# Optimization experiments

Hardware: AMD Instinct MI355X
Metric: run time of the kernel (lower is better)

## Reference

```python
import jax, jax.numpy as jnp
import numpy as np

GRAVITY = 9.81
W_INERTIA = 1.0
W_GRAVITY = 0.01
W_STRAIN = 1.0

V = 500_000
E = 2_000_000


def setup_inputs() -> dict:
    key = jax.random.key(0)
    ks = jax.random.split(key, 7)
    pos_next = jax.random.normal(ks[0], (V, 3), dtype=jnp.float32)
    pos_curr = jax.random.normal(ks[1], (V, 3), dtype=jnp.float32)
    pos_prev = jax.random.normal(ks[2], (V, 3), dtype=jnp.float32)
    mass = jax.random.uniform(ks[3], (V, 1), dtype=jnp.float32)
    elements = jax.random.randint(ks[4], (E, 4), 0, V, dtype=jnp.int64)
    rest_volumes = jax.random.uniform(ks[5], (E,), dtype=jnp.float32)
    rest_inv = jax.random.normal(ks[6], (E, 3, 3), dtype=jnp.float32)
    lam = jnp.float32(1.0)
    mu = jnpp_one = jnp.float32(1.0)
    return {
        "pos_next": pos_next, "pos_curr": pos_curr, "pos_prev": pos_prev,
        "mass": mass, "elements": elements, "rest_volumes": rest_volumes,
        "rest_inv": rest_inv, "lam": lam, "mu": mu,
    }


def _det3(F):
    # F: (E, 3, 3)
    return (F[:, 0, 0] * (F[:, 1, 1] * F[:, 2, 2] - F[:, 1, 2] * F[:, 2, 1])
            - F[:, 0, 1] * (F[:, 1, 0] * F[:, 2, 2] - F[:, 1, 2] * F[:, 2, 0])
            + F[:, 0, 2] * (F[:, 1, 0] * F[:, 2, 1] - F[:, 1, 1] * F[:, 2, 0]))


def _physics_loss(pos_next, pos_curr, pos_prev, mass, elements, rest_volumes, rest_inv, lam, mu):
    # Inertia: mean over all V*3 entries of 0.5 * m * a^2
    accel = pos_next + pos_prev - 2.0 * pos_curr          # (V, 3)
    inertia = 0.5 * jnp.mean(mass * accel * accel)
    # Gravity: -mean(m * g * y)
    gravity = -jnp.mean(mass * GRAVITY * pos_curr[:, 1:2])
    # Strain (Neo-Hookean) on pos_next
    v = pos_next[elements]                                 # (E, 4, 3)
    Ds = jnp.stack([v[:, 1] - v[:, 0], v[:, 2] - v[:, 0], v[:, 3] - v[:, 0]], axis=-1)  # (E,3,3)
    F_def = jnp.einsum('eij,ejk->eik', Ds, rest_inv)       # (E, 3, 3)
    det_F = jnp.maximum(_det3(F_def), 1e-8)
    log_det = jnp.log(det_F)
    tr_FtF = jnp.sum(F_def * F_def, axis=(1, 2))           # trace(F^T F) = ||F||_F^2
    psi = 0.5 * lam * log_det ** 2 - mu * log_det + 0.5 * mu * (tr_FtF - 3.0)
    strain = jnp.mean(psi * rest_volumes)
    return W_INERTIA * inertia + W_GRAVITY * gravity + W_STRAIN * strain


def reference(pos_next, pos_curr, pos_prev, mass, elements, rest_volumes, rest_inv, lam, mu):
    return _physics_loss(pos_next, pos_curr, pos_prev, mass, elements, rest_volumes, rest_inv, lam, mu)
```

## Files before the change

### kernel.cpp

```cpp
#include <hip/hip_runtime.h>

#define GRAVITY_F 9.81f

__device__ __forceinline__ float blockReduceSum(float val) {
    #pragma unroll
    for (int off = 32; off > 0; off >>= 1)
        val += __shfl_down(val, off, 64);
    __shared__ float smem[16];
    const int lane = threadIdx.x & 63;
    const int wave = threadIdx.x >> 6;
    if (lane == 0) smem[wave] = val;
    __syncthreads();
    const int nwaves = (blockDim.x + 63) >> 6;
    val = 0.0f;
    if (wave == 0) {
        if (lane < nwaves) val = smem[lane];
        #pragma unroll
        for (int off = 8; off > 0; off >>= 1)
            val += __shfl_down(val, off, 64);
    }
    return val;
}

__global__ void fused_kernel(const float* __restrict__ pn,
                             const float* __restrict__ pc,
                             const float* __restrict__ pp,
                             const float* __restrict__ mass,
                             const int*   __restrict__ elems,
                             const float* __restrict__ vols,
                             const float* __restrict__ rinv,
                             const float* __restrict__ lam_p,
                             const float* __restrict__ mu_p,
                             float* __restrict__ partials,
                             double* __restrict__ acc,
                             int V, int E,
                             float sI, float sG, float sS) {
    const int i = blockIdx.x * blockDim.x + threadIdx.x;
    float local = 0.0f;

    if (i < V) {
        const int v = i;
        const float m  = mass[v];
        const float p0 = pc[3 * v + 0];
        const float y  = pc[3 * v + 1];
        const float p2 = pc[3 * v + 2];
        const float a0 = pn[3 * v + 0] + pp[3 * v + 0] - 2.0f * p0;
        const float a1 = pn[3 * v + 1] + pp[3 * v + 1] - 2.0f * y;
        const float a2 = pn[3 * v + 2] + pp[3 * v + 2] - 2.0f * p2;
        local = sI * (m * (a0 * a0 + a1 * a1 + a2 * a2)) + sG * (m * y);
    } else if (i < V + E) {
        const int e = i - V;
        const float lam = lam_p[0];
        const float mu  = mu_p[0];
        const int4 idx = ((const int4*)elems)[e];
        const float* v0 = pn + 3 * (size_t)idx.x;
        const float* v1 = pn + 3 * (size_t)idx.y;
        const float* v2 = pn + 3 * (size_t)idx.z;
        const float* v3 = pn + 3 * (size_t)idx.w;

        float d[3][3];
        #pragma unroll
        for (int r = 0; r < 3; ++r) {
            const float b = v0[r];
            d[r][0] = v1[r] - b;
            d[r][1] = v2[r] - b;
            d[r][2] = v3[r] - b;
        }

        const float* R = rinv + 9 * (size_t)e;
        float F[3][3];
        #pragma unroll
        for (int r = 0; r < 3; ++r) {
            #pragma unroll
            for (int k = 0; k < 3; ++k) {
                F[r][k] = d[r][0] * R[0 * 3 + k]
                        + d[r][1] * R[1 * 3 + k]
                        + d[r][2] * R[2 * 3 + k];
            }
        }

        const float det = F[0][0] * (F[1][1] * F[2][2] - F[1][2] * F[2][1])
                        - F[0][1] * (F[1][0] * F[2][2] - F[1][2] * F[2][0])
                        + F[0][2] * (F[1][0] * F[2][1] - F[1][1] * F[2][0]);
        const float ld = logf(fmaxf(det, 1e-8f));
        float tr = 0.0f;
        #pragma unroll
        for (int r = 0; r < 3; ++r)
            #pragma unroll
            for (int k = 0; k < 3; ++k)
                tr += F[r][k] * F[r][k];

        const float psi = 0.5f * lam * ld * ld - mu * ld + 0.5f * mu * (tr - 3.0f);
        local = sS * (psi * vols[e]);
    }

    const float tot = blockReduceSum(local);
    if (threadIdx.x == 0) {
        if (partials) partials[blockIdx.x] = tot;
        else atomicAdd(acc, (double)tot);
    }
}

__global__ void reduce_kernel(const float* __restrict__ partials, int n,
                              float* __restrict__ out) {
    double s = 0.0;
    for (int i = threadIdx.x; i < n; i += blockDim.x)
        s += (double)partials[i];
    __shared__ double sm[256];
    sm[threadIdx.x] = s;
    __syncthreads();
    #pragma unroll
    for (int off = 128; off > 0; off >>= 1) {
        if (threadIdx.x < off) sm[threadIdx.x] += sm[threadIdx.x + off];
        __syncthreads();
    }
    if (threadIdx.x == 0) out[0] = (float)sm[0];
}

__global__ void init_acc_kernel(double* acc) {
    if (threadIdx.x == 0 && blockIdx.x == 0) acc[0] = 0.0;
}
__global__ void finalize_kernel(const double* __restrict__ acc,
                                float* __restrict__ out) {
    if (threadIdx.x == 0 && blockIdx.x == 0) out[0] = (float)acc[0];
}

extern "C" void kernel_launch(void* const* d_in, const int* in_sizes, int n_in,
                              void* d_out, int out_size, void* d_ws, size_t ws_size,
                              hipStream_t stream) {
    const float* pos_next = (const float*)d_in[0];
    const float* pos_curr = (const float*)d_in[1];
    const float* pos_prev = (const float*)d_in[2];
    const float* mass     = (const float*)d_in[3];
    const int*   elements = (const int*)d_in[4];
    const float* rest_vol = (const float*)d_in[5];
    const float* rest_inv = (const float*)d_in[6];
    const float* lam_p    = (const float*)d_in[7];
    const float* mu_p     = (const float*)d_in[8];
    float* out = (float*)d_out;

    const int V = in_sizes[3];
    const int E = in_sizes[5];

    const float sI = 0.5f / (3.0f * (float)V);
    const float sG = -0.01f * GRAVITY_F / (float)V;
    const float sS = 1.0f / (float)E;

    const int block = 256;
    const int nitems = V + E;
    const int grid = (nitems + block - 1) / block;

    const bool use_partials = ws_size >= (size_t)grid * sizeof(float) + 64;

    if (use_partials) {
        float* partials = (float*)d_ws;
        fused_kernel<<<grid, block, 0, stream>>>(pos_next, pos_curr, pos_prev,
                                                 mass, elements, rest_vol,
                                                 rest_inv, lam_p, mu_p,
                                                 partials, nullptr,
                                                 V, E, sI, sG, sS);
        reduce_kernel<<<1, 256, 0, stream>>>(partials, grid, out);
    } else {
        double* acc = (double*)d_ws;
        init_acc_kernel<<<1, 1, 0, stream>>>(acc);
        fused_kernel<<<grid, block, 0, stream>>>(pos_next, pos_curr, pos_prev,
                                                 mass, elements, rest_vol,
                                                 rest_inv, lam_p, mu_p,
                                                 nullptr, acc,
                                                 V, E, sI, sG, sS);
        finalize_kernel<<<1, 1, 0, stream>>>(acc, out);
    }
}
```

Baseline: 229.9 us.

## Split blocks by role, process two elements per thread, use nontemporal streaming loads

Vertex and element work now go to separate, block-aligned ranges, so no wave is split between the two paths. Each element-block thread handles two tetrahedra and issues both index loads before computing, which raises memory-level parallelism for the gathers. Streaming inputs (mass, pos_curr, pos_prev, indices, volumes, rest_inv) use nontemporal loads so they do not evict pos_next from cache, since pos_next is gathered. The atomic fallback path is removed, so the code now assumes the workspace is large enough to hold the per-block partials.

```diff
diff --git a/kernel.cpp b/kernel.cpp
--- a/kernel.cpp
+++ b/kernel.cpp
@@ -1,6 +1,8 @@
 #include <hip/hip_runtime.h>
 
 #define GRAVITY_F 9.81f
+
+typedef int v4i __attribute__((ext_vector_type(4)));
 
 __device__ __forceinline__ float blockReduceSum(float val) {
     #pragma unroll
@@ -22,6 +24,51 @@
     return val;
 }
 
+__device__ __forceinline__ float elem_term(const float* __restrict__ pn,
+                                           const v4i idx,
+                                           const float vol,
+                                           const float* __restrict__ R,
+                                           float lam, float mu, float sS) {
+    float x0[3], x1[3], x2[3], x3[3];
+    const float* v0 = pn + 3 * (size_t)idx.x;
+    const float* v1 = pn + 3 * (size_t)idx.y;
+    const float* v2 = pn + 3 * (size_t)idx.z;
+    const float* v3 = pn + 3 * (size_t)idx.w;
+    #pragma unroll
+    for (int r = 0; r < 3; ++r) { x0[r] = v0[r]; x1[r] = v1[r]; x2[r] = v2[r]; x3[r] = v3[r]; }
+
+    float Rv[9];
+    #pragma unroll
+    for (int k = 0; k < 9; ++k) Rv[k] = __builtin_nontemporal_load(R + k);
+
+    float d[3][3];
+    #pragma unroll
+    for (int r = 0; r < 3; ++r) {
+        d[r][0] = x1[r] - x0[r];
+        d[r][1] = x2[r] - x0[r];
+        d[r][2] = x3[r] - x0[r];
+    }
+    float F[3][3];
+    #pragma unroll
+    for (int r = 0; r < 3; ++r) {
+        #pragma unroll
+        for (int k = 0; k < 3; ++k)
+            F[r][k] = d[r][0] * Rv[0 * 3 + k] + d[r][1] * Rv[1 * 3 + k] + d[r][2] * Rv[2 * 3 + k];
+    }
+    const float det = F[0][0] * (F[1][1] * F[2][2] - F[1][2] * F[2][1])
+                    - F[0][1] * (F[1][0] * F[2][2] - F[1][2] * F[2][0])
+                    + F[0][2] * (F[1][0] * F[2][1] - F[1][1] * F[2][0]);
+    const float ld = logf(fmaxf(det, 1e-8f));
+    float tr = 0.0f;
+    #pragma unroll
+    for (int r = 0; r < 3; ++r)
+        #pragma unroll
+        for (int k = 0; k < 3; ++k)
+            tr += F[r][k] * F[r][k];
+    const float psi = 0.5f * lam * ld * ld - mu * ld + 0.5f * mu * (tr - 3.0f);
+    return sS * (psi * vol);
+}
+
 __global__ void fused_kernel(const float* __restrict__ pn,
                              const float* __restrict__ pc,
                              const float* __restrict__ pp,
@@ -32,73 +79,48 @@
                              const float* __restrict__ lam_p,
                              const float* __restrict__ mu_p,
                              float* __restrict__ partials,
-                             double* __restrict__ acc,
-                             int V, int E,
+                             int V, int E, int Vblocks,
                              float sI, float sG, float sS) {
-    const int i = blockIdx.x * blockDim.x + threadIdx.x;
     float local = 0.0f;
 
-    if (i < V) {
-        const int v = i;
-        const float m  = mass[v];
-        const float p0 = pc[3 * v + 0];
-        const float y  = pc[3 * v + 1];
-        const float p2 = pc[3 * v + 2];
-        const float a0 = pn[3 * v + 0] + pp[3 * v + 0] - 2.0f * p0;
-        const float a1 = pn[3 * v + 1] + pp[3 * v + 1] - 2.0f * y;
-        const float a2 = pn[3 * v + 2] + pp[3 * v + 2] - 2.0f * p2;
-        local = sI * (m * (a0 * a0 + a1 * a1 + a2 * a2)) + sG * (m * y);
-    } else if (i < V + E) {
-        const int e = i - V;
+    if ((int)blockIdx.x < Vblocks) {
+        const int v = blockIdx.x * blockDim.x + threadIdx.x;
+        if (v < V) {
+            const float m  = __builtin_nontemporal_load(mass + v);
+            const float p0 = __builtin_nontemporal_load(pc + 3 * v + 0);
+            const float y  = __builtin_nontemporal_load(pc + 3 * v + 1);
+            const float p2 = __builtin_nontemporal_load(pc + 3 * v + 2);
+            const float n0 = pn[3 * v + 0];
+            const float n1 = pn[3 * v + 1];
+            const float n2 = pn[3 * v + 2];
+            const float q0 = __builtin_nontemporal_load(pp + 3 * v + 0);
+            const float q1 = __builtin_nontemporal_load(pp + 3 * v + 1);
+            const float q2 = __builtin_nontemporal_load(pp + 3 * v + 2);
+            const float a0 = n0 + q0 - 2.0f * p0;
+            const float a1 = n1 + q1 - 2.0f * y;
+            const float a2 = n2 + q2 - 2.0f * p2;
+            local = sI * (m * (a0 * a0 + a1 * a1 + a2 * a2)) + sG * (m * y);
+        }
+    } else {
         const float lam = lam_p[0];
         const float mu  = mu_p[0];
-        const int4 idx = ((const int4*)elems)[e];
-        const float* v0 = pn + 3 * (size_t)idx.x;
-        const float* v1 = pn + 3 * (size_t)idx.y;
-        const float* v2 = pn + 3 * (size_t)idx.z;
-        const float* v3 = pn + 3 * (size_t)idx.w;
+        const int base = (blockIdx.x - Vblocks) * (2 * blockDim.x);
+        const int e0 = base + threadIdx.x;
+        const int e1 = e0 + blockDim.x;
 
-        float d[3][3];
-        #pragma unroll
-        for (int r = 0; r < 3; ++r) {
-            const float b = v0[r];
-            d[r][0] = v1[r] - b;
-            d[r][1] = v2[r] - b;
-            d[r][2] = v3[r] - b;
-        }
-
-        const float* R = rinv + 9 * (size_t)e;
-        float F[3][3];
-        #pragma unroll
-        for (int r = 0; r < 3; ++r) {
-            #pragma unroll
-            for (int k = 0; k < 3; ++k) {
-                F[r][k] = d[r][0] * R[0 * 3 + k]
-                        + d[r][1] * R[1 * 3 + k]
-                        + d[r][2] * R[2 * 3 + k];
-            }
-        }
-
-        const float det = F[0][0] * (F[1][1] * F[2][2] - F[1][2] * F[2][1])
-                        - F[0][1] * (F[1][0] * F[2][2] - F[1][2] * F[2][0])
-                        + F[0][2] * (F[1][0] * F[2][1] - F[1][1] * F[2][0]);
-        const float ld = logf(fmaxf(det, 1e-8f));
-        float tr = 0.0f;
-        #pragma unroll
-        for (int r = 0; r < 3; ++r)
-            #pragma unroll
-            for (int k = 0; k < 3; ++k)
-                tr += F[r][k] * F[r][k];
-
-        const float psi = 0.5f * lam * ld * ld - mu * ld + 0.5f * mu * (tr - 3.0f);
-        local = sS * (psi * vols[e]);
+        v4i idx0 = (v4i)(0), idx1 = (v4i)(0);
+        float vol0 = 0.0f, vol1 = 0.0f;
+        const bool ok0 = e0 < E, ok1 = e1 < E;
+        if (ok0) { idx0 = __builtin_nontemporal_load(((const v4i*)elems) + e0);
+                   vol0 = __builtin_nontemporal_load(vols + e0); }
+        if (ok1) { idx1 = __builtin_nontemporal_load(((const v4i*)elems) + e1);
+                   vol1 = __builtin_nontemporal_load(vols + e1); }
+        if (ok0) local += elem_term(pn, idx0, vol0, rinv + 9 * (size_t)e0, lam, mu, sS);
+        if (ok1) local += elem_term(pn, idx1, vol1, rinv + 9 * (size_t)e1, lam, mu, sS);
     }
 
     const float tot = blockReduceSum(local);
-    if (threadIdx.x == 0) {
-        if (partials) partials[blockIdx.x] = tot;
-        else atomicAdd(acc, (double)tot);
-    }
+    if (threadIdx.x == 0) partials[blockIdx.x] = tot;
 }
 
 __global__ void reduce_kernel(const float* __restrict__ partials, int n,
@@ -115,14 +137,6 @@
         __syncthreads();
     }
     if (threadIdx.x == 0) out[0] = (float)sm[0];
-}
-
-__global__ void init_acc_kernel(double* acc) {
-    if (threadIdx.x == 0 && blockIdx.x == 0) acc[0] = 0.0;
-}
-__global__ void finalize_kernel(const double* __restrict__ acc,
-                                float* __restrict__ out) {
-    if (threadIdx.x == 0 && blockIdx.x == 0) out[0] = (float)acc[0];
 }
 
 extern "C" void kernel_launch(void* const* d_in, const int* in_sizes, int n_in,
@@ -147,27 +161,16 @@
     const float sS = 1.0f / (float)E;
 
     const int block = 256;
-    const int nitems = V + E;
-    const int grid = (nitems + block - 1) / block;
+    const int Vblocks = (V + block - 1) / block;
+    const int Eblocks = (E + 2 * block - 1) / (2 * block);
+    const int grid = Vblocks + Eblocks;
 
-    const bool use_partials = ws_size >= (size_t)grid * sizeof(float) + 64;
+    float* partials = (float*)d_ws;
 
-    if (use_partials) {
-        float* partials = (float*)d_ws;
-        fused_kernel<<<grid, block, 0, stream>>>(pos_next, pos_curr, pos_prev,
-                                                 mass, elements, rest_vol,
-                                                 rest_inv, lam_p, mu_p,
-                                                 partials, nullptr,
-                                                 V, E, sI, sG, sS);
-        reduce_kernel<<<1, 256, 0, stream>>>(partials, grid, out);
-    } else {
-        double* acc = (double*)d_ws;
-        init_acc_kernel<<<1, 1, 0, stream>>>(acc);
-        fused_kernel<<<grid, block, 0, stream>>>(pos_next, pos_curr, pos_prev,
-                                                 mass, elements, rest_vol,
-                                                 rest_inv, lam_p, mu_p,
-                                                 nullptr, acc,
-                                                 V, E, sI, sG, sS);
-        finalize_kernel<<<1, 1, 0, stream>>>(acc, out);
-    }
+    fused_kernel<<<grid, block, 0, stream>>>(pos_next, pos_curr, pos_prev,
+                                             mass, elements, rest_vol,
+                                             rest_inv, lam_p, mu_p,
+                                             partials, V, E, Vblocks,
+                                             sI, sG, sS);
+    reduce_kernel<<<1, 256, 0, stream>>>(partials, grid, out);
 }
```

New measurement: 226.7 us. Within noise of the previous version (-1.4%).
